# Kernel tuning notes

Measured on AMD Instinct MI355X. Metric: run time of the kernel, lower is better.

Reference implementation:

```python
import jax, jax.numpy as jnp
import numpy as np

N_NODES = 50000
N_EDGES = 800000
F = 64      # node feature channels (irreps_out = 64x0e)
L = 4       # edge spherical-harmonic dim (lmax=1)
R = 8       # radial basis size
H = 64      # radial MLP hidden
AVG_NUM_NEIGHBOURS = 16.0


def setup_inputs() -> dict:
    key = jax.random.key(0)
    ks = jax.random.split(key, 10)
    node_features = jax.random.normal(ks[0], (N_NODES, F), jnp.float32)
    edge_features = jax.random.normal(ks[1], (N_EDGES, L), jnp.float32)
    radial_embedding = jax.random.uniform(ks[2], (N_EDGES, R), jnp.float32)
    senders = jax.random.randint(ks[3], (N_EDGES,), 0, N_NODES)
    receivers = jax.random.randint(ks[4], (N_EDGES,), 0, N_NODES)
    edge_mask = jnp.ones((N_EDGES,), jnp.bool_)
    W_up = jax.random.normal(ks[5], (F, F), jnp.float32) / np.sqrt(F)
    W1 = jax.random.normal(ks[6], (R, H), jnp.float32) / np.sqrt(R)
    W2 = jax.random.normal(ks[7], (H, H), jnp.float32) / np.sqrt(H)
    W3 = jax.random.normal(ks[8], (H, F * L), jnp.float32) / np.sqrt(H)
    W_down = jax.random.normal(ks[9], (F, F), jnp.float32) / np.sqrt(F)
    return dict(node_features=node_features, edge_features=edge_features,
                radial_embedding=radial_embedding, senders=senders,
                receivers=receivers, edge_mask=edge_mask,
                W_up=W_up, W1=W1, W2=W2, W3=W3, W_down=W_down)


def reference(node_features, edge_features, radial_embedding, senders,
              receivers, edge_mask, W_up, W1, W2, W3, W_down):
    n_nodes = node_features.shape[0]
    # linear_up
    x = node_features @ W_up  # [N, F]
    # radial MLP -> per-edge, per-(channel, l) tensor-product path weights
    h = jax.nn.swish(radial_embedding @ W1)
    h = jax.nn.swish(h @ W2)
    w = (h @ W3).reshape(-1, F, L)  # [E, F, L]
    # gather sender features, weighted tensor product with edge attrs,
    # contracted over the edge-attribute (spherical-harmonic) axis
    x_s = x[senders]  # [E, F]
    msg = jnp.einsum('ef,el,efl->ef', x_s, edge_features, w)  # [E, F]
    msg = jnp.where(edge_mask[:, None], msg, jnp.zeros((), msg.dtype))
    # scatter-add to receivers and normalize
    agg = jax.ops.segment_sum(msg, receivers, num_segments=n_nodes)
    agg = agg / AVG_NUM_NEIGHBOURS
    # linear_down
    return agg @ W_down
```

## Files before the change

### kernel.cpp

```cpp
#include <hip/hip_runtime.h>
#include <hip/hip_bf16.h>

typedef _Float16 half8 __attribute__((ext_vector_type(8)));
typedef _Float16 half4v __attribute__((ext_vector_type(4)));
typedef _Float16 half2v __attribute__((ext_vector_type(2)));
typedef float f32x4 __attribute__((ext_vector_type(4)));

#define NN 50000
#define NE 800000

__device__ __forceinline__ float swishf(float v) {
  return v * __builtin_amdgcn_rcpf(1.f + __expf(-v));
}

__global__ void pack_kernel(const float* __restrict__ W3, const float* __restrict__ W2,
                            _Float16* __restrict__ w3p, _Float16* __restrict__ w2p) {
  const int b = blockIdx.x, tid = threadIdx.x;
  if (b < 8) {
    int t = b * 256 + tid;
    int lane = t & 63, nt = (t >> 6) & 3, ks = t >> 8;
    int f = 16 * nt + (lane & 15);
    int jb = 32 * ks + 8 * (lane >> 4);
#pragma unroll
    for (int u = 0; u < 8; ++u) {
      int j = jb + u;
      w3p[t * 8 + u] = (_Float16)W3[(j >> 2) * 256 + 4 * f + (j & 3)];
    }
  } else {
    int t = (b - 8) * 256 + tid;
    if (t < 512) {
      int lane = t & 63, nt = (t >> 6) & 3, kk = t >> 8;
      int c = 16 * nt + (lane & 15);
      int kb = 32 * kk + 8 * (lane >> 4);
#pragma unroll
      for (int u = 0; u < 8; ++u)
        w2p[t * 8 + u] = (_Float16)W2[(kb + u) * 64 + c];
    }
  }
}

__global__ __launch_bounds__(256)
void linear_up_kernel(const float* __restrict__ X, const float* __restrict__ W,
                      _Float16* __restrict__ Y) {
  int gid = blockIdx.x * 256 + (int)threadIdx.x;
  int row = gid >> 6;
  int lane = threadIdx.x & 63;
  const float* xr = X + (long)row * 64;
  float acc = 0.f;
#pragma unroll
  for (int k = 0; k < 64; ++k) acc = fmaf(xr[k], W[k * 64 + lane], acc);
  Y[(long)row * 64 + lane] = (_Float16)acc;
}

__global__ void hist_kernel(const int* __restrict__ rcv, int* __restrict__ deg) {
  int e = blockIdx.x * 256 + threadIdx.x;
  if (e < NE) atomicAdd(&deg[rcv[e]], 1);
}

__global__ __launch_bounds__(256)
void scan1_kernel(const int* __restrict__ deg, int* __restrict__ bsum) {
  __shared__ int s[256];
  int gid = blockIdx.x * 256 + threadIdx.x;
  s[threadIdx.x] = (gid < NN) ? deg[gid] : 0;
  __syncthreads();
  for (int d = 128; d > 0; d >>= 1) {
    if (threadIdx.x < d) s[threadIdx.x] += s[threadIdx.x + d];
    __syncthreads();
  }
  if (threadIdx.x == 0) bsum[blockIdx.x] = s[0];
}

__global__ __launch_bounds__(256)
void scan2_kernel(const int* __restrict__ bsum, int* __restrict__ boff) {
  __shared__ int s[256];
  int t = threadIdx.x;
  int v = (t < 196) ? bsum[t] : 0;
  s[t] = v;
  __syncthreads();
  for (int d = 1; d < 256; d <<= 1) {
    int x = (t >= d) ? s[t - d] : 0;
    __syncthreads();
    s[t] += x;
    __syncthreads();
  }
  boff[t] = s[t] - v;
}

__global__ __launch_bounds__(256)
void scan3_kernel(const int* __restrict__ deg, const int* __restrict__ boff,
                  int* __restrict__ pos, int* __restrict__ cur) {
  __shared__ int s[256];
  int t = threadIdx.x, gid = blockIdx.x * 256 + t;
  int v = (gid < NN) ? deg[gid] : 0;
  s[t] = v;
  __syncthreads();
  for (int d = 1; d < 256; d <<= 1) {
    int x = (t >= d) ? s[t - d] : 0;
    __syncthreads();
    s[t] += x;
    __syncthreads();
  }
  int ex = s[t] - v + boff[blockIdx.x];
  if (gid < NN) {
    pos[gid] = ex;
    cur[gid] = ex;
    if (gid == NN - 1) pos[NN] = ex + v;
  }
}

__global__ __launch_bounds__(256, 6)
void fused_tp_kernel(const float* __restrict__ rad, const float* __restrict__ ef,
                     const _Float16* __restrict__ xup, const int* __restrict__ snd,
                     const int* __restrict__ rcv, const int* __restrict__ msk,
                     const float* __restrict__ W1,
                     const _Float16* __restrict__ w2p, const _Float16* __restrict__ w3p,
                     int* __restrict__ cur, _Float16* __restrict__ msg) {
  __shared__ float    s_r[64][9];
  __shared__ float    s_ef[64][4];
  __shared__ _Float16 s_xs[64][72];
  __shared__ _Float16 s_hp[64][72];
  __shared__ int      s_slot[64];

  const int t = threadIdx.x;
  const long e0 = (long)blockIdx.x * 64;
  const int w = t >> 6, lane = t & 63, m = lane & 15, g = lane >> 4;

  for (int i = t; i < 512; i += 256) s_r[i >> 3][i & 7] = rad[e0 * 8 + i];
  s_ef[t >> 2][t & 3] = ef[e0 * 4 + t];
  if (t < 64) s_slot[t] = atomicAdd(&cur[rcv[e0 + t]], 1);
  {
    const int e = t >> 2, q = t & 3;
    const int sn = snd[e0 + e];
    const int mk = msk[e0 + e];
    uint4 v0 = {0, 0, 0, 0}, v1 = {0, 0, 0, 0};
    if (mk) {
      const uint4* src = reinterpret_cast<const uint4*>(xup + (long)sn * 64 + q * 16);
      v0 = src[0]; v1 = src[1];
    }
    *reinterpret_cast<uint4*>(&s_xs[e][q * 16]) = v0;
    *reinterpret_cast<uint4*>(&s_xs[e][q * 16 + 8]) = v1;
  }
  __syncthreads();

  const int e_m = w * 16 + m;

  float rv[8];
#pragma unroll
  for (int k = 0; k < 8; ++k) rv[k] = s_r[e_m][k];

  half8 afrag[2];
#pragma unroll
  for (int kk = 0; kk < 2; ++kk) {
    float acc[8];
#pragma unroll
    for (int u = 0; u < 8; ++u) acc[u] = 0.f;
#pragma unroll
    for (int k = 0; k < 8; ++k) {
      const float4 wa = *reinterpret_cast<const float4*>(W1 + k * 64 + 32 * kk + 8 * g);
      const float4 wb = *reinterpret_cast<const float4*>(W1 + k * 64 + 32 * kk + 8 * g + 4);
      acc[0] = fmaf(rv[k], wa.x, acc[0]);
      acc[1] = fmaf(rv[k], wa.y, acc[1]);
      acc[2] = fmaf(rv[k], wa.z, acc[2]);
      acc[3] = fmaf(rv[k], wa.w, acc[3]);
      acc[4] = fmaf(rv[k], wb.x, acc[4]);
      acc[5] = fmaf(rv[k], wb.y, acc[5]);
      acc[6] = fmaf(rv[k], wb.z, acc[6]);
      acc[7] = fmaf(rv[k], wb.w, acc[7]);
    }
#pragma unroll
    for (int u = 0; u < 8; ++u) afrag[kk][u] = (_Float16)swishf(acc[u]);
  }

  {
    f32x4 acc2[4];
#pragma unroll
    for (int nt = 0; nt < 4; ++nt) acc2[nt] = (f32x4){0.f, 0.f, 0.f, 0.f};
#pragma unroll
    for (int kk = 0; kk < 2; ++kk) {
#pragma unroll
      for (int nt = 0; nt < 4; ++nt) {
        half8 bfr = *reinterpret_cast<const half8*>(w2p + ((size_t)(kk * 4 + nt) * 64 + lane) * 8);
        acc2[nt] = __builtin_amdgcn_mfma_f32_16x16x32_f16(afrag[kk], bfr, acc2[nt], 0, 0, 0);
      }
    }
    const int col = lane & 15, rg = lane >> 4;
    const int pbase = 16 * ((col >> 1) & 3) + 2 * (col >> 3) + (col & 1);
#pragma unroll
    for (int nt = 0; nt < 4; ++nt) {
      const int pos = pbase + 4 * nt;
#pragma unroll
      for (int i = 0; i < 4; ++i) {
        const int erow = w * 16 + rg * 4 + i;
        s_hp[erow][pos] = (_Float16)swishf(acc2[nt][i]);
      }
    }
  }

  {
    const _Float16* hrow = &s_hp[e_m][g * 16];
    half8 hlo = *reinterpret_cast<const half8*>(hrow);
    half8 hhi = *reinterpret_cast<const half8*>(hrow + 8);

    _Float16 efh[4];
#pragma unroll
    for (int l = 0; l < 4; ++l) efh[l] = (_Float16)s_ef[e_m][l];

    f32x4 acc[4];
#pragma unroll
    for (int nt = 0; nt < 4; ++nt) acc[nt] = (f32x4){0.f, 0.f, 0.f, 0.f};

#pragma unroll
    for (int ks = 0; ks < 8; ++ks) {
      const _Float16 h0  = (ks < 4) ? hlo[2 * ks]     : hhi[2 * (ks - 4)];
      const _Float16 h1v = (ks < 4) ? hlo[2 * ks + 1] : hhi[2 * (ks - 4) + 1];
      half8 a;
#pragma unroll
      for (int l = 0; l < 4; ++l) {
        a[l]     = h0  * efh[l];
        a[4 + l] = h1v * efh[l];
      }
#pragma unroll
      for (int nt = 0; nt < 4; ++nt) {
        half8 bfr = *reinterpret_cast<const half8*>(w3p + ((size_t)(ks * 4 + nt) * 64 + lane) * 8);
        acc[nt] = __builtin_amdgcn_mfma_f32_16x16x32_f16(a, bfr, acc[nt], 0, 0, 0);
      }
    }

    const int col = lane & 15, rg = lane >> 4;
#pragma unroll
    for (int nt = 0; nt < 4; ++nt) {
      const int f = nt * 16 + col;
#pragma unroll
      for (int i = 0; i < 4; ++i) {
        const int e_row = w * 16 + rg * 4 + i;
        s_hp[e_row][f] = (_Float16)(acc[nt][i] * (float)s_xs[e_row][f]);
      }
    }
  }

  {
    const int e = t >> 2, q = t & 3;
    uint4 v0 = *reinterpret_cast<const uint4*>(&s_hp[e][q * 16]);
    uint4 v1 = *reinterpret_cast<const uint4*>(&s_hp[e][q * 16 + 8]);
    _Float16* dst = msg + (long)s_slot[e] * 64 + q * 16;
    *reinterpret_cast<uint4*>(dst) = v0;
    *reinterpret_cast<uint4*>(dst + 8) = v1;
  }
}

__global__ __launch_bounds__(256, 8)
void gather_down_kernel(const _Float16* __restrict__ msg, const int* __restrict__ pos,
                        const float* __restrict__ W_dn, float* __restrict__ out) {
  __shared__ int   s_pos[17];
  __shared__ float s_agg[16][65];

  const int t = threadIdx.x;
  const int node0 = blockIdx.x * 16;

  if (t < 17) s_pos[t] = pos[node0 + t];
  __syncthreads();

  const int tg = t >> 4, tl = t & 15;
  float a0 = 0.f, a1 = 0.f, a2 = 0.f, a3 = 0.f;
  for (int a = s_pos[tg]; a < s_pos[tg + 1]; ++a) {
    half4v v = *reinterpret_cast<const half4v*>(msg + (long)a * 64 + tl * 4);
    a0 += (float)v[0]; a1 += (float)v[1]; a2 += (float)v[2]; a3 += (float)v[3];
  }
  s_agg[tg][tl * 4 + 0] = a0;
  s_agg[tg][tl * 4 + 1] = a1;
  s_agg[tg][tl * 4 + 2] = a2;
  s_agg[tg][tl * 4 + 3] = a3;
  __syncthreads();

  {
    const int r = t >> 4, c0 = (t & 15) * 4;
    float b0 = 0.f, b1 = 0.f, b2 = 0.f, b3 = 0.f;
    for (int k = 0; k < 64; ++k) {
      const float x = s_agg[r][k];
      const float4 wv = *reinterpret_cast<const float4*>(W_dn + k * 64 + c0);
      b0 = fmaf(x, wv.x, b0);
      b1 = fmaf(x, wv.y, b1);
      b2 = fmaf(x, wv.z, b2);
      b3 = fmaf(x, wv.w, b3);
    }
    float4 o = { b0 * 0.0625f, b1 * 0.0625f, b2 * 0.0625f, b3 * 0.0625f };
    *reinterpret_cast<float4*>(out + (long)(node0 + r) * 64 + c0) = o;
  }
}

extern "C" void kernel_launch(void* const* d_in, const int* in_sizes, int n_in,
                              void* d_out, int out_size, void* d_ws, size_t ws_size,
                              hipStream_t stream) {
  const float* nf   = (const float*)d_in[0];
  const float* ef   = (const float*)d_in[1];
  const float* rad  = (const float*)d_in[2];
  const int*   snd  = (const int*)d_in[3];
  const int*   rcv  = (const int*)d_in[4];
  const int*   msk  = (const int*)d_in[5];
  const float* W_up = (const float*)d_in[6];
  const float* W1   = (const float*)d_in[7];
  const float* W2   = (const float*)d_in[8];
  const float* W3   = (const float*)d_in[9];
  const float* W_dn = (const float*)d_in[10];
  float* out = (float*)d_out;

  _Float16* msg  = (_Float16*)d_ws;
  _Float16* xbuf = msg + (size_t)NE * 64;
  _Float16* w3p  = xbuf + (size_t)NN * 64;
  _Float16* w2p  = w3p + 2048 * 8;
  int*      deg  = (int*)(w2p + 512 * 8);
  int*      pos  = deg + NN;
  int*      cur  = pos + NN + 1;
  int*      bsum = cur + NN;
  int*      boff = bsum + 256;

  hipMemsetAsync(deg, 0, (size_t)NN * sizeof(int), stream);

  hist_kernel<<<NE / 256, 256, 0, stream>>>(rcv, deg);
  scan1_kernel<<<196, 256, 0, stream>>>(deg, bsum);
  scan2_kernel<<<1, 256, 0, stream>>>(bsum, boff);
  scan3_kernel<<<196, 256, 0, stream>>>(deg, boff, pos, cur);

  pack_kernel<<<10, 256, 0, stream>>>(W3, W2, w3p, w2p);
  linear_up_kernel<<<(NN * 64) / 256, 256, 0, stream>>>(nf, W_up, xbuf);

  fused_tp_kernel<<<NE / 64, 256, 0, stream>>>(rad, ef, xbuf, snd, rcv, msk,
                                               W1, w2p, w3p, cur, msg);

  gather_down_kernel<<<NN / 16, 256, 0, stream>>>(msg, pos, W_dn, out);
}
```

Measured before the change: 266.2 us.

## Process 32 edges per wave in fused TP kernel and drop block barrier

Each block now handles 128 edges, each wave 32 edges as two MFMA row tiles. The W2 and W3 B-fragments loaded once per wave now feed two MFMAs each, halving weight-fragment traffic per edge. Each wave loads and consumes only its own edges' data, so the __syncthreads is removed and radial inputs are read straight from global into registers instead of through shared memory. In exchange, register use and LDS per block rise, so launch bounds drop to 4 blocks per CU, lowering occupancy for a kernel that is largely bound by gather latency.

```diff
diff --git a/kernel.cpp b/kernel.cpp
--- a/kernel.cpp
+++ b/kernel.cpp
@@ -3,7 +3,6 @@
 
 typedef _Float16 half8 __attribute__((ext_vector_type(8)));
 typedef _Float16 half4v __attribute__((ext_vector_type(4)));
-typedef _Float16 half2v __attribute__((ext_vector_type(2)));
 typedef float f32x4 __attribute__((ext_vector_type(4)));
 
 #define NN 50000
@@ -108,79 +107,97 @@
   }
 }
 
-__global__ __launch_bounds__(256, 6)
+__global__ __launch_bounds__(256, 4)
 void fused_tp_kernel(const float* __restrict__ rad, const float* __restrict__ ef,
                      const _Float16* __restrict__ xup, const int* __restrict__ snd,
                      const int* __restrict__ rcv, const int* __restrict__ msk,
                      const float* __restrict__ W1,
                      const _Float16* __restrict__ w2p, const _Float16* __restrict__ w3p,
                      int* __restrict__ cur, _Float16* __restrict__ msg) {
-  __shared__ float    s_r[64][9];
-  __shared__ float    s_ef[64][4];
-  __shared__ _Float16 s_xs[64][72];
-  __shared__ _Float16 s_hp[64][72];
-  __shared__ int      s_slot[64];
+  __shared__ float    s_ef[128][4];
+  __shared__ _Float16 s_xs[128][72];
+  __shared__ _Float16 s_hp[128][72];
+  __shared__ int      s_slot[128];
 
   const int t = threadIdx.x;
-  const long e0 = (long)blockIdx.x * 64;
+  const long e0 = (long)blockIdx.x * 128;
   const int w = t >> 6, lane = t & 63, m = lane & 15, g = lane >> 4;
-
-  for (int i = t; i < 512; i += 256) s_r[i >> 3][i & 7] = rad[e0 * 8 + i];
-  s_ef[t >> 2][t & 3] = ef[e0 * 4 + t];
-  if (t < 64) s_slot[t] = atomicAdd(&cur[rcv[e0 + t]], 1);
-  {
-    const int e = t >> 2, q = t & 3;
+  const int ew0 = 32 * w;
+
+  {
+    const float2 e2 = *reinterpret_cast<const float2*>(ef + (e0 + ew0) * 4 + lane * 2);
+    const int rr = ew0 + (lane >> 1), rc = 2 * (lane & 1);
+    s_ef[rr][rc] = e2.x;
+    s_ef[rr][rc + 1] = e2.y;
+    if (lane < 32) s_slot[ew0 + lane] = atomicAdd(&cur[rcv[e0 + ew0 + lane]], 1);
+    const int e = ew0 + (lane >> 1), q2 = lane & 1;
     const int sn = snd[e0 + e];
     const int mk = msk[e0 + e];
-    uint4 v0 = {0, 0, 0, 0}, v1 = {0, 0, 0, 0};
+    uint4 v0 = {0,0,0,0}, v1 = {0,0,0,0}, v2 = {0,0,0,0}, v3 = {0,0,0,0};
     if (mk) {
-      const uint4* src = reinterpret_cast<const uint4*>(xup + (long)sn * 64 + q * 16);
-      v0 = src[0]; v1 = src[1];
-    }
-    *reinterpret_cast<uint4*>(&s_xs[e][q * 16]) = v0;
-    *reinterpret_cast<uint4*>(&s_xs[e][q * 16 + 8]) = v1;
-  }
-  __syncthreads();
-
-  const int e_m = w * 16 + m;
-
-  float rv[8];
-#pragma unroll
-  for (int k = 0; k < 8; ++k) rv[k] = s_r[e_m][k];
-
-  half8 afrag[2];
+      const uint4* src = reinterpret_cast<const uint4*>(xup + (long)sn * 64 + q2 * 32);
+      v0 = src[0]; v1 = src[1]; v2 = src[2]; v3 = src[3];
+    }
+    uint4* dst = reinterpret_cast<uint4*>(&s_xs[e][q2 * 32]);
+    dst[0] = v0; dst[1] = v1; dst[2] = v2; dst[3] = v3;
+  }
+
+  const int em0 = ew0 + m;
+  const int em1 = ew0 + 16 + m;
+
+  float rv0[8], rv1[8];
+  {
+    const float4 a = *reinterpret_cast<const float4*>(rad + (e0 + em0) * 8);
+    const float4 b = *reinterpret_cast<const float4*>(rad + (e0 + em0) * 8 + 4);
+    const float4 c = *reinterpret_cast<const float4*>(rad + (e0 + em1) * 8);
+    const float4 d = *reinterpret_cast<const float4*>(rad + (e0 + em1) * 8 + 4);
+    rv0[0]=a.x; rv0[1]=a.y; rv0[2]=a.z; rv0[3]=a.w;
+    rv0[4]=b.x; rv0[5]=b.y; rv0[6]=b.z; rv0[7]=b.w;
+    rv1[0]=c.x; rv1[1]=c.y; rv1[2]=c.z; rv1[3]=c.w;
+    rv1[4]=d.x; rv1[5]=d.y; rv1[6]=d.z; rv1[7]=d.w;
+  }
+
+  half8 af0[2], af1[2];
 #pragma unroll
   for (int kk = 0; kk < 2; ++kk) {
-    float acc[8];
-#pragma unroll
-    for (int u = 0; u < 8; ++u) acc[u] = 0.f;
+    float a0[8], a1[8];
+#pragma unroll
+    for (int u = 0; u < 8; ++u) { a0[u] = 0.f; a1[u] = 0.f; }
 #pragma unroll
     for (int k = 0; k < 8; ++k) {
       const float4 wa = *reinterpret_cast<const float4*>(W1 + k * 64 + 32 * kk + 8 * g);
       const float4 wb = *reinterpret_cast<const float4*>(W1 + k * 64 + 32 * kk + 8 * g + 4);
-      acc[0] = fmaf(rv[k], wa.x, acc[0]);
-      acc[1] = fmaf(rv[k], wa.y, acc[1]);
-      acc[2] = fmaf(rv[k], wa.z, acc[2]);
-      acc[3] = fmaf(rv[k], wa.w, acc[3]);
-      acc[4] = fmaf(rv[k], wb.x, acc[4]);
-      acc[5] = fmaf(rv[k], wb.y, acc[5]);
-      acc[6] = fmaf(rv[k], wb.z, acc[6]);
-      acc[7] = fmaf(rv[k], wb.w, acc[7]);
-    }
-#pragma unroll
-    for (int u = 0; u < 8; ++u) afrag[kk][u] = (_Float16)swishf(acc[u]);
-  }
-
-  {
-    f32x4 acc2[4];
-#pragma unroll
-    for (int nt = 0; nt < 4; ++nt) acc2[nt] = (f32x4){0.f, 0.f, 0.f, 0.f};
+      a0[0] = fmaf(rv0[k], wa.x, a0[0]);  a1[0] = fmaf(rv1[k], wa.x, a1[0]);
+      a0[1] = fmaf(rv0[k], wa.y, a0[1]);  a1[1] = fmaf(rv1[k], wa.y, a1[1]);
+      a0[2] = fmaf(rv0[k], wa.z, a0[2]);  a1[2] = fmaf(rv1[k], wa.z, a1[2]);
+      a0[3] = fmaf(rv0[k], wa.w, a0[3]);  a1[3] = fmaf(rv1[k], wa.w, a1[3]);
+      a0[4] = fmaf(rv0[k], wb.x, a0[4]);  a1[4] = fmaf(rv1[k], wb.x, a1[4]);
+      a0[5] = fmaf(rv0[k], wb.y, a0[5]);  a1[5] = fmaf(rv1[k], wb.y, a1[5]);
+      a0[6] = fmaf(rv0[k], wb.z, a0[6]);  a1[6] = fmaf(rv1[k], wb.z, a1[6]);
+      a0[7] = fmaf(rv0[k], wb.w, a0[7]);  a1[7] = fmaf(rv1[k], wb.w, a1[7]);
+    }
+#pragma unroll
+    for (int u = 0; u < 8; ++u) {
+      af0[kk][u] = (_Float16)swishf(a0[u]);
+      af1[kk][u] = (_Float16)swishf(a1[u]);
+    }
+  }
+
+  {
+    half8 bw[8];
+#pragma unroll
+    for (int i = 0; i < 8; ++i)
+      bw[i] = *reinterpret_cast<const half8*>(w2p + ((size_t)i * 64 + lane) * 8);
+
+    f32x4 A0[4], A1[4];
+#pragma unroll
+    for (int nt = 0; nt < 4; ++nt) { A0[nt] = (f32x4){0.f,0.f,0.f,0.f}; A1[nt] = (f32x4){0.f,0.f,0.f,0.f}; }
 #pragma unroll
     for (int kk = 0; kk < 2; ++kk) {
 #pragma unroll
       for (int nt = 0; nt < 4; ++nt) {
-        half8 bfr = *reinterpret_cast<const half8*>(w2p + ((size_t)(kk * 4 + nt) * 64 + lane) * 8);
-        acc2[nt] = __builtin_amdgcn_mfma_f32_16x16x32_f16(afrag[kk], bfr, acc2[nt], 0, 0, 0);
+        A0[nt] = __builtin_amdgcn_mfma_f32_16x16x32_f16(af0[kk], bw[kk * 4 + nt], A0[nt], 0, 0, 0);
+        A1[nt] = __builtin_amdgcn_mfma_f32_16x16x32_f16(af1[kk], bw[kk * 4 + nt], A1[nt], 0, 0, 0);
       }
     }
     const int col = lane & 15, rg = lane >> 4;
@@ -190,39 +207,55 @@
       const int pos = pbase + 4 * nt;
 #pragma unroll
       for (int i = 0; i < 4; ++i) {
-        const int erow = w * 16 + rg * 4 + i;
-        s_hp[erow][pos] = (_Float16)swishf(acc2[nt][i]);
-      }
-    }
-  }
-
-  {
-    const _Float16* hrow = &s_hp[e_m][g * 16];
-    half8 hlo = *reinterpret_cast<const half8*>(hrow);
-    half8 hhi = *reinterpret_cast<const half8*>(hrow + 8);
-
-    _Float16 efh[4];
-#pragma unroll
-    for (int l = 0; l < 4; ++l) efh[l] = (_Float16)s_ef[e_m][l];
-
-    f32x4 acc[4];
-#pragma unroll
-    for (int nt = 0; nt < 4; ++nt) acc[nt] = (f32x4){0.f, 0.f, 0.f, 0.f};
+        const int r0 = ew0 + rg * 4 + i;
+        s_hp[r0][pos]      = (_Float16)swishf(A0[nt][i]);
+        s_hp[r0 + 16][pos] = (_Float16)swishf(A1[nt][i]);
+      }
+    }
+  }
+
+  {
+    const _Float16* hr0 = &s_hp[em0][g * 16];
+    const _Float16* hr1 = &s_hp[em1][g * 16];
+    half8 hlo0 = *reinterpret_cast<const half8*>(hr0);
+    half8 hhi0 = *reinterpret_cast<const half8*>(hr0 + 8);
+    half8 hlo1 = *reinterpret_cast<const half8*>(hr1);
+    half8 hhi1 = *reinterpret_cast<const half8*>(hr1 + 8);
+
+    _Float16 ef0[4], ef1[4];
+#pragma unroll
+    for (int l = 0; l < 4; ++l) {
+      ef0[l] = (_Float16)s_ef[em0][l];
+      ef1[l] = (_Float16)s_ef[em1][l];
+    }
+
+    f32x4 c0[4], c1[4];
+#pragma unroll
+    for (int nt = 0; nt < 4; ++nt) { c0[nt] = (f32x4){0.f,0.f,0.f,0.f}; c1[nt] = (f32x4){0.f,0.f,0.f,0.f}; }
 
 #pragma unroll
     for (int ks = 0; ks < 8; ++ks) {
-      const _Float16 h0  = (ks < 4) ? hlo[2 * ks]     : hhi[2 * (ks - 4)];
-      const _Float16 h1v = (ks < 4) ? hlo[2 * ks + 1] : hhi[2 * (ks - 4) + 1];
-      half8 a;
+      half8 bfr[4];
+#pragma unroll
+      for (int nt = 0; nt < 4; ++nt)
+        bfr[nt] = *reinterpret_cast<const half8*>(w3p + ((size_t)(ks * 4 + nt) * 64 + lane) * 8);
+
+      const _Float16 p0  = (ks < 4) ? hlo0[2 * ks]     : hhi0[2 * (ks - 4)];
+      const _Float16 p1  = (ks < 4) ? hlo0[2 * ks + 1] : hhi0[2 * (ks - 4) + 1];
+      const _Float16 q0  = (ks < 4) ? hlo1[2 * ks]     : hhi1[2 * (ks - 4)];
+      const _Float16 q1  = (ks < 4) ? hlo1[2 * ks + 1] : hhi1[2 * (ks - 4) + 1];
+      half8 a0, a1;
 #pragma unroll
       for (int l = 0; l < 4; ++l) {
-        a[l]     = h0  * efh[l];
-        a[4 + l] = h1v * efh[l];
+        a0[l]     = p0 * ef0[l];
+        a0[4 + l] = p1 * ef0[l];
+        a1[l]     = q0 * ef1[l];
+        a1[4 + l] = q1 * ef1[l];
       }
 #pragma unroll
       for (int nt = 0; nt < 4; ++nt) {
-        half8 bfr = *reinterpret_cast<const half8*>(w3p + ((size_t)(ks * 4 + nt) * 64 + lane) * 8);
-        acc[nt] = __builtin_amdgcn_mfma_f32_16x16x32_f16(a, bfr, acc[nt], 0, 0, 0);
+        c0[nt] = __builtin_amdgcn_mfma_f32_16x16x32_f16(a0, bfr[nt], c0[nt], 0, 0, 0);
+        c1[nt] = __builtin_amdgcn_mfma_f32_16x16x32_f16(a1, bfr[nt], c1[nt], 0, 0, 0);
       }
     }
 
@@ -232,19 +265,19 @@
       const int f = nt * 16 + col;
 #pragma unroll
       for (int i = 0; i < 4; ++i) {
-        const int e_row = w * 16 + rg * 4 + i;
-        s_hp[e_row][f] = (_Float16)(acc[nt][i] * (float)s_xs[e_row][f]);
-      }
-    }
-  }
-
-  {
-    const int e = t >> 2, q = t & 3;
-    uint4 v0 = *reinterpret_cast<const uint4*>(&s_hp[e][q * 16]);
-    uint4 v1 = *reinterpret_cast<const uint4*>(&s_hp[e][q * 16 + 8]);
-    _Float16* dst = msg + (long)s_slot[e] * 64 + q * 16;
-    *reinterpret_cast<uint4*>(dst) = v0;
-    *reinterpret_cast<uint4*>(dst + 8) = v1;
+        const int r0 = ew0 + rg * 4 + i;
+        s_hp[r0][f]      = (_Float16)(c0[nt][i] * (float)s_xs[r0][f]);
+        s_hp[r0 + 16][f] = (_Float16)(c1[nt][i] * (float)s_xs[r0 + 16][f]);
+      }
+    }
+  }
+
+  {
+    const int e = ew0 + (lane >> 1), q2 = lane & 1;
+    const uint4* src = reinterpret_cast<const uint4*>(&s_hp[e][q2 * 32]);
+    uint4 v0 = src[0], v1 = src[1], v2 = src[2], v3 = src[3];
+    uint4* dst = reinterpret_cast<uint4*>(msg + (long)s_slot[e] * 64 + q2 * 32);
+    dst[0] = v0; dst[1] = v1; dst[2] = v2; dst[3] = v3;
   }
 }
 
@@ -324,8 +357,8 @@
   pack_kernel<<<10, 256, 0, stream>>>(W3, W2, w3p, w2p);
   linear_up_kernel<<<(NN * 64) / 256, 256, 0, stream>>>(nf, W_up, xbuf);
 
-  fused_tp_kernel<<<NE / 64, 256, 0, stream>>>(rad, ef, xbuf, snd, rcv, msk,
-                                               W1, w2p, w3p, cur, msg);
+  fused_tp_kernel<<<NE / 128, 256, 0, stream>>>(rad, ef, xbuf, snd, rcv, msk,
+                                                W1, w2p, w3p, cur, msg);
 
   gather_down_kernel<<<NN / 16, 256, 0, stream>>>(msg, pos, W_dn, out);
 }
```

Measured after the change: 245.5 us. 1.08x faster.
